# Kernel tuning notes

Measured on AMD Instinct MI355X. Metric: run time of the kernel, lower is better.

Reference implementation:

```python
import jax, jax.numpy as jnp
import numpy as np

B, S, D, H = 2, 2048, 1024, 16
HD = D // H  # 64
SOFT_CAP = 50.0
MAX_WAVELENGTH = 10000.0


def apply_rope(x, positions, head_dim):
    # x: [B,S,H,hd], positions: [B,S]
    fraction = 2.0 * jnp.arange(head_dim // 2, dtype=jnp.float32) / head_dim
    timescale = MAX_WAVELENGTH ** fraction                      # [hd/2]
    sinusoid = positions.astype(jnp.float32)[..., None] / timescale  # [B,S,hd/2]
    sin = jnp.sin(sinusoid)[..., None, :]                       # [B,S,1,hd/2]
    cos = jnp.cos(sinusoid)[..., None, :]
    first, second = jnp.split(x, 2, axis=-1)
    out = jnp.concatenate(
        [first * cos - second * sin, second * cos + first * sin], axis=-1)
    return out.astype(x.dtype)


def setup_inputs() -> dict:
    key = jax.random.key(0)
    k1, k2, k3 = jax.random.split(key, 3)
    inputs = jax.random.normal(k1, (B, S, D), jnp.float32)
    segment_positions = jnp.tile(jnp.arange(S, dtype=jnp.int32), (B, 1))
    mask = jnp.tril(jnp.ones((S, S), dtype=bool))[None, None]   # causal [1,1,S,S]
    w_in = jax.random.normal(k2, (D, H, 3 * HD), jnp.float32) * 0.02
    w_out = jax.random.normal(k3, (H, HD, D), jnp.float32) * 0.02
    return {"inputs": inputs, "segment_positions": segment_positions,
            "mask": mask, "w_in": w_in, "w_out": w_out}


def reference(inputs, segment_positions, mask, w_in, w_out):
    # fused QKV projection: [B,S,H,3*hd]
    proj = jnp.einsum('bsd,dhe->bshe', inputs, w_in)
    q, k, v = jnp.split(proj, 3, axis=-1)
    q = apply_rope(q, segment_positions, HD)
    k = apply_rope(k, segment_positions, HD)
    q = q / jnp.sqrt(jnp.float32(HD))
    attn = jnp.einsum('bqhd,bkhd->bhqk', q, k)                  # [B,H,S,S]
    big_neg = jnp.finfo(jnp.float32).min
    attn = jnp.where(mask, attn, big_neg)
    attn = jnp.tanh(attn / SOFT_CAP) * SOFT_CAP                 # soft-cap AFTER mask
    attn = jax.nn.softmax(attn, axis=-1)
    x = jnp.einsum('bhqk,bkhd->bqhd', attn, v)
    return jnp.einsum('bqhd,hdo->bqo', x, w_out)
```

## Files before the change

### kernel.cpp

```cpp
#include <hip/hip_runtime.h>
#include <math.h>

#define BB 2
#define SS 2048
#define DD 1024
#define HH 16
#define HDIM 64
#define BS (BB*SS)
#define NQKV (HH*3*HDIM)
#define PERHEAD ((size_t)SS*HDIM)

typedef __attribute__((ext_vector_type(8))) short bf16x8;
typedef __attribute__((ext_vector_type(4))) short bf16x4;
typedef __attribute__((ext_vector_type(4))) float f32x4;

typedef const __attribute__((address_space(1))) unsigned int ga_u32;
typedef __attribute__((address_space(3))) unsigned int lds_u32;

__device__ inline short f2bf(float x) {
    union { float f; unsigned u; } v; v.f = x;
    unsigned r = v.u + 0x7FFF + ((v.u >> 16) & 1);
    return (short)(r >> 16);
}

__device__ inline void gl_lds16(const void* g, void* l) {
    __builtin_amdgcn_global_load_lds((ga_u32*)g, (lds_u32*)l, 16, 0, 0);
}

__device__ inline f32x4 mfma16(bf16x4 a, bf16x4 b, f32x4 c) {
#if __has_builtin(__builtin_amdgcn_mfma_f32_16x16x16bf16_1k)
    return __builtin_amdgcn_mfma_f32_16x16x16bf16_1k(a, b, c, 0, 0, 0);
#else
    f32x4 d;
    asm("v_mfma_f32_16x16x16_bf16 %0, %1, %2, %3"
        : "=v"(d) : "v"(a), "v"(b), "v"(c));
    return d;
#endif
}

__global__ __launch_bounds__(256)
void prep_kernel(const float* __restrict__ A, unsigned short* __restrict__ Ab,
                 const int* __restrict__ pos, float2* __restrict__ tab)
{
    int bid = blockIdx.x, t = threadIdx.x;
    if (bid < 4096) {
        int i = (bid * 256 + t) * 4;
        float4 v = *(const float4*)&A[i];
        ushort4 o;
        o.x = (unsigned short)f2bf(v.x); o.y = (unsigned short)f2bf(v.y);
        o.z = (unsigned short)f2bf(v.z); o.w = (unsigned short)f2bf(v.w);
        *(ushort4*)&Ab[i] = o;
    } else {
        int idx = (bid - 4096) * 256 + t;
        int i = idx & 31, s = (idx >> 5) & 2047, b = idx >> 16;
        float p  = (float)pos[b * SS + s];
        float ts = powf(10000.0f, (float)i / 32.0f);
        float sn, cs;
        sincosf(p / ts, &sn, &cs);
        tab[idx] = make_float2(cs, sn);
    }
}

__global__ __launch_bounds__(256)
void transpose2_bf16(const float* __restrict__ Win, unsigned short* __restrict__ Wtin,
                     const float* __restrict__ Wout, unsigned short* __restrict__ Wtout)
{
    __shared__ float tile[64][65];
    int id = blockIdx.x;
    const float* W; unsigned short* Wt; int K, N, tx, ty;
    if (id < 768) { W = Win;  Wt = Wtin;  K = DD; N = NQKV; tx = id % 48; ty = id / 48; }
    else { id -= 768; W = Wout; Wt = Wtout; K = DD; N = DD;  tx = id % 16; ty = id / 16; }
    const int k0 = ty * 64, n0 = tx * 64;
    const int t = threadIdx.x;
    #pragma unroll
    for (int i = 0; i < 4; ++i) {
        int lin = t + 256 * i;
        int r = lin >> 4, c4 = (lin & 15) << 2;
        float4 v = *(const float4*)&W[(size_t)(k0 + r) * N + n0 + c4];
        tile[r][c4] = v.x; tile[r][c4 + 1] = v.y;
        tile[r][c4 + 2] = v.z; tile[r][c4 + 3] = v.w;
    }
    __syncthreads();
    #pragma unroll
    for (int i = 0; i < 4; ++i) {
        int lin = t + 256 * i;
        int n = lin >> 4, c4 = (lin & 15) << 2;
        ushort4 o;
        o.x = (unsigned short)f2bf(tile[c4 + 0][n]);
        o.y = (unsigned short)f2bf(tile[c4 + 1][n]);
        o.z = (unsigned short)f2bf(tile[c4 + 2][n]);
        o.w = (unsigned short)f2bf(tile[c4 + 3][n]);
        *(ushort4*)&Wt[(size_t)(n0 + n) * K + k0 + c4] = o;
    }
}

template<int QKV, int NT>
__global__ __launch_bounds__(256)
void gemm_mfma(const unsigned short* __restrict__ A,
               const unsigned short* __restrict__ Bt,
               float* __restrict__ C,
               unsigned short* __restrict__ Qb, unsigned short* __restrict__ Kb,
               unsigned short* __restrict__ Vb,
               const float2* __restrict__ tab,
               int M, int N, int K)
{
    __shared__ __align__(16) unsigned short As[128 * 32];
    __shared__ __align__(16) unsigned short Bs[NT * 32 * 32];
    const int t = threadIdx.x;
    const int wave = t >> 6, lane = t & 63;
    const int quad = lane >> 4, lc = lane & 15;
    const int bm = blockIdx.y * 128, bn = blockIdx.x * (NT * 32);
    const int wr = wave >> 1, wc = wave & 1;

    const int cb   = blockIdx.x * 2 + wc;
    const int h    = QKV ? (cb / 3) : 0;
    const int part = QKV ? (cb % 3) : 0;
    const bool vswap = QKV && (part == 2);

    const int r4 = lane >> 2;
    const int sc = (lane & 3) ^ ((lane >> 3) & 3);
    const unsigned short* aptr0 = A + (size_t)(bm + wave * 32 + r4) * K + sc * 8;
    const unsigned short* aptr1 = aptr0 + (size_t)16 * K;
    unsigned short* alds0 = &As[(wave * 32) * 32];
    unsigned short* alds1 = alds0 + 16 * 32;
    const unsigned short* bptr0 = Bt + (size_t)(bn + wave * (NT * 8) + r4) * K + sc * 8;
    const unsigned short* bptr1 = bptr0 + (size_t)16 * K;
    unsigned short* blds0 = &Bs[(wave * (NT * 8)) * 32];
    unsigned short* blds1 = blds0 + 16 * 32;

    const int cx = quad ^ ((lc >> 1) & 3);

    f32x4 acc[4][NT] = {};

    for (int k0 = 0; k0 < K; k0 += 32) {
        gl_lds16(aptr0 + k0, alds0);
        gl_lds16(aptr1 + k0, alds1);
        gl_lds16(bptr0 + k0, blds0);
        if (NT == 4) gl_lds16(bptr1 + k0, blds1);
        __syncthreads();

        bf16x8 af[4], bfr[NT];
        #pragma unroll
        for (int rt = 0; rt < 4; ++rt)
            af[rt] = *(const bf16x8*)&As[(wr * 64 + rt * 16 + lc) * 32 + cx * 8];
        #pragma unroll
        for (int nt = 0; nt < NT; ++nt)
            bfr[nt] = *(const bf16x8*)&Bs[(wc * (NT * 16) + nt * 16 + lc) * 32 + cx * 8];
        if (vswap) {
            #pragma unroll
            for (int rt = 0; rt < 4; ++rt)
                #pragma unroll
                for (int nt = 0; nt < NT; ++nt)
                    acc[rt][nt] = __builtin_amdgcn_mfma_f32_16x16x32_bf16(
                        bfr[nt], af[rt], acc[rt][nt], 0, 0, 0);
        } else {
            #pragma unroll
            for (int rt = 0; rt < 4; ++rt)
                #pragma unroll
                for (int nt = 0; nt < NT; ++nt)
                    acc[rt][nt] = __builtin_amdgcn_mfma_f32_16x16x32_bf16(
                        af[rt], bfr[nt], acc[rt][nt], 0, 0, 0);
        }
        __syncthreads();
    }

    if (QKV) {
        if (part == 2) {
            #pragma unroll
            for (int rt = 0; rt < 4; ++rt) {
                int m = bm + wr * 64 + rt * 16 + lc;
                int b = m >> 11, s = m & 2047;
                #pragma unroll
                for (int nt = 0; nt < 4; ++nt) {
                    #pragma unroll
                    for (int reg = 0; reg < 4; ++reg) {
                        int hd = nt * 16 + quad * 4 + reg;
                        Vb[(((size_t)(b * HH + h)) * HDIM + hd) * SS + s] =
                            (unsigned short)f2bf(acc[rt][nt][reg]);
                    }
                }
            }
        } else {
            unsigned short* dst = part == 0 ? Qb : Kb;
            const float scale = part == 0 ? 0.125f : 1.0f;
            #pragma unroll
            for (int rt = 0; rt < 4; ++rt) {
                #pragma unroll
                for (int reg = 0; reg < 4; ++reg) {
                    int m = bm + wr * 64 + rt * 16 + quad * 4 + reg;
                    int b = m >> 11, s = m & 2047;
                    size_t rowbase = (((size_t)(b * HH + h)) * SS + s) * HDIM;
                    #pragma unroll
                    for (int nt = 0; nt < 2; ++nt) {
                        int i = nt * 16 + lc;
                        float2 cssn = tab[((size_t)(b * SS + s)) * 32 + i];
                        float first  = acc[rt][nt][reg];
                        float second = acc[rt][nt + 2][reg];
                        dst[rowbase + i] =
                            (unsigned short)f2bf((first * cssn.x - second * cssn.y) * scale);
                        dst[rowbase + i + 32] =
                            (unsigned short)f2bf((second * cssn.x + first * cssn.y) * scale);
                    }
                }
            }
        }
    } else {
        #pragma unroll
        for (int rt = 0; rt < 4; ++rt)
            #pragma unroll
            for (int reg = 0; reg < 4; ++reg) {
                int m = bm + wr * 64 + rt * 16 + quad * 4 + reg;
                #pragma unroll
                for (int nt = 0; nt < NT; ++nt) {
                    int n = bn + wc * (NT * 16) + nt * 16 + lc;
                    C[(size_t)m * N + n] = acc[rt][nt][reg];
                }
            }
    }
}

__global__ __launch_bounds__(256)
void attn_mfma_kernel(const unsigned short* __restrict__ Qb,
                      const unsigned short* __restrict__ Kb,
                      const unsigned short* __restrict__ Vb,
                      unsigned short* __restrict__ Xb)
{
    __shared__ __align__(16) unsigned short Ks[2][64 * 64];
    __shared__ __align__(16) unsigned short Vs[2][64 * 64];

    const int t    = threadIdx.x;
    const int wave = t >> 6, lane = t & 63;
    const int quad = lane >> 4, lc = lane & 15;
    const int qt   = 31 - (blockIdx.x >> 5);
    const int bh   = blockIdx.x & 31;
    const int b    = bh >> 4, h = bh & 15;

    const unsigned short* Kbase = Kb + (size_t)bh * PERHEAD;
    const unsigned short* Vbase = Vb + (size_t)bh * PERHEAD;

    const int r8 = lane >> 3, c8 = lane & 7, gcs = c8 ^ r8;

    const unsigned short* Qbase =
        Qb + ((size_t)bh * SS + (size_t)(qt * 64 + wave * 16)) * HDIM;
    bf16x8 qf[2];
    qf[0] = *(const bf16x8*)&Qbase[lc * HDIM + quad * 8];
    qf[1] = *(const bf16x8*)&Qbase[lc * HDIM + 32 + quad * 8];

    f32x4 O[4] = {{0,0,0,0},{0,0,0,0},{0,0,0,0},{0,0,0,0}};
    float l = 0.0f;

    {
        const unsigned short* ks = Kbase + (size_t)(wave * 16 + r8) * HDIM + gcs * 8;
        gl_lds16(ks,            &Ks[0][(wave * 16)     * 64]);
        gl_lds16(ks + 8 * HDIM, &Ks[0][(wave * 16 + 8) * 64]);
        const unsigned short* vs = Vbase + (size_t)(wave * 16 + r8) * SS + gcs * 8;
        gl_lds16(vs,          &Vs[0][(wave * 16)     * 64]);
        gl_lds16(vs + 8 * SS, &Vs[0][(wave * 16 + 8) * 64]);
    }

    for (int kt = 0; kt <= qt; ++kt) {
        __syncthreads();
        const int buf = kt & 1;
        if (kt < qt) {
            const int nb = buf ^ 1;
            const unsigned short* ks =
                Kbase + (size_t)((kt + 1) * 64 + wave * 16 + r8) * HDIM + gcs * 8;
            gl_lds16(ks,            &Ks[nb][(wave * 16)     * 64]);
            gl_lds16(ks + 8 * HDIM, &Ks[nb][(wave * 16 + 8) * 64]);
            const unsigned short* vs =
                Vbase + (size_t)(wave * 16 + r8) * SS + (kt + 1) * 64 + gcs * 8;
            gl_lds16(vs,          &Vs[nb][(wave * 16)     * 64]);
            gl_lds16(vs + 8 * SS, &Vs[nb][(wave * 16 + 8) * 64]);
        }

        f32x4 St[4];
        #pragma unroll
        for (int kg = 0; kg < 4; ++kg) {
            St[kg] = (f32x4){0.f, 0.f, 0.f, 0.f};
            #pragma unroll
            for (int khd = 0; khd < 2; ++khd) {
                int pc = ((khd << 2) | quad) ^ (lc & 7);
                bf16x8 kf = *(const bf16x8*)&Ks[buf][(kg * 16 + lc) * 64 + pc * 8];
                St[kg] = __builtin_amdgcn_mfma_f32_16x16x32_bf16(
                    kf, qf[khd], St[kg], 0, 0, 0);
            }
        }

        const bool diag = (kt == qt);
        bf16x4 pf[4];
        #pragma unroll
        for (int kg = 0; kg < 4; ++kg) {
            #pragma unroll
            for (int reg = 0; reg < 4; ++reg) {
                float s  = St[kg][reg];
                float s2 = s * s;
                float u  = fmaf(s2 * s, -1.92359246e-4f, s * 1.44269504f);
                float p  = __builtin_amdgcn_exp2f(u);
                if (diag && (kg * 16 + quad * 4 + reg > wave * 16 + lc)) p = 0.f;
                l += p;
                pf[kg][reg] = f2bf(p);
            }
        }

        #pragma unroll
        for (int g = 0; g < 4; ++g) {
            #pragma unroll
            for (int kg = 0; kg < 4; ++kg) {
                int pc2 = (kg * 2 + (quad >> 1)) ^ (lc & 7);
                bf16x4 vf = *(const bf16x4*)
                    &Vs[buf][(g * 16 + lc) * 64 + pc2 * 8 + (quad & 1) * 4];
                O[g] = mfma16(pf[kg], vf, O[g]);
            }
        }
    }

    l += __shfl_xor(l, 16);
    l += __shfl_xor(l, 32);
    #pragma unroll
    for (int reg = 0; reg < 4; ++reg) {
        float lq  = __shfl(l, quad * 4 + reg);
        float inv = __builtin_amdgcn_rcpf(lq);
        int q_g = qt * 64 + wave * 16 + quad * 4 + reg;
        size_t base = ((size_t)b * SS + q_g) * DD + h * HDIM;
        #pragma unroll
        for (int g = 0; g < 4; ++g)
            Xb[base + g * 16 + lc] = (unsigned short)f2bf(O[g][reg] * inv);
    }
}

extern "C" void kernel_launch(void* const* d_in, const int* in_sizes, int n_in,
                              void* d_out, int out_size, void* d_ws, size_t ws_size,
                              hipStream_t stream)
{
    const float* inputs = (const float*)d_in[0];
    const int*   pos    = (const int*)d_in[1];
    const float* w_in   = (const float*)d_in[3];
    const float* w_out  = (const float*)d_in[4];
    float* out = (float*)d_out;

    const size_t NELT = (size_t)BB * HH * SS * HDIM;
    unsigned short* Ab     = (unsigned short*)d_ws;
    unsigned short* Wt_in  = Ab + NELT;
    unsigned short* Wt_out = Wt_in + (size_t)NQKV * DD;
    unsigned short* Qb     = Wt_out + (size_t)DD * DD;
    unsigned short* Kb     = Qb + NELT;
    unsigned short* Vb     = Kb + NELT;
    unsigned short* Xb     = Vb + NELT;
    float2*         tab    = (float2*)(Xb + NELT);

    dim3 blk(256);
    prep_kernel<<<dim3(4096 + 512), blk, 0, stream>>>(inputs, Ab, pos, tab);
    transpose2_bf16<<<dim3(1024), blk, 0, stream>>>(w_in, Wt_in, w_out, Wt_out);
    gemm_mfma<1, 4><<<dim3(NQKV / 128, BS / 128), blk, 0, stream>>>(
        Ab, Wt_in, nullptr, Qb, Kb, Vb, tab, BS, NQKV, DD);
    attn_mfma_kernel<<<dim3(32 * BB * HH), blk, 0, stream>>>(Qb, Kb, Vb, Xb);
    gemm_mfma<0, 2><<<dim3(DD / 64, BS / 128), blk, 0, stream>>>(
        Xb, Wt_out, out, nullptr, nullptr, nullptr, nullptr, BS, DD, DD);
}
```

Before: 191.1 us.

## Merge prep kernels and compute softmax row sums via MFMA in attention

Folds the weight transpose kernel into the input-conversion/rope-table kernel, saving one launch. In the attention inner loop, the bf16 conversion becomes a round-half-up plus byte-permute pack, and the softmax denominator is accumulated with an MFMA against a ones vector instead of scalar adds and cross-lane shuffles. The denominator now sums the bf16-rounded probabilities, which matches the values fed to the PV product. The merged setup kernel reserves shared memory for every block, including the conversion blocks that do not use it, which may lower their occupancy.

After: 188.0 us (median of 2 runs). About the same (-1.6%).

```diff
diff --git a/kernel.cpp b/kernel.cpp
--- a/kernel.cpp
+++ b/kernel.cpp
@@ -39,9 +39,12 @@
 }
 
 __global__ __launch_bounds__(256)
-void prep_kernel(const float* __restrict__ A, unsigned short* __restrict__ Ab,
-                 const int* __restrict__ pos, float2* __restrict__ tab)
+void setup_kernel(const float* __restrict__ A, unsigned short* __restrict__ Ab,
+                  const int* __restrict__ pos, float2* __restrict__ tab,
+                  const float* __restrict__ Win, unsigned short* __restrict__ Wtin,
+                  const float* __restrict__ Wout, unsigned short* __restrict__ Wtout)
 {
+    __shared__ float tile[64][65];
     int bid = blockIdx.x, t = threadIdx.x;
     if (bid < 4096) {
         int i = (bid * 256 + t) * 4;
@@ -50,7 +53,9 @@
         o.x = (unsigned short)f2bf(v.x); o.y = (unsigned short)f2bf(v.y);
         o.z = (unsigned short)f2bf(v.z); o.w = (unsigned short)f2bf(v.w);
         *(ushort4*)&Ab[i] = o;
-    } else {
+        return;
+    }
+    if (bid < 4608) {
         int idx = (bid - 4096) * 256 + t;
         int i = idx & 31, s = (idx >> 5) & 2047, b = idx >> 16;
         float p  = (float)pos[b * SS + s];
@@ -58,20 +63,12 @@
         float sn, cs;
         sincosf(p / ts, &sn, &cs);
         tab[idx] = make_float2(cs, sn);
-    }
-}
-
-__global__ __launch_bounds__(256)
-void transpose2_bf16(const float* __restrict__ Win, unsigned short* __restrict__ Wtin,
-                     const float* __restrict__ Wout, unsigned short* __restrict__ Wtout)
-{
-    __shared__ float tile[64][65];
-    int id = blockIdx.x;
+        return;
+    }
     const float* W; unsigned short* Wt; int K, N, tx, ty;
-    if (id < 768) { W = Win;  Wt = Wtin;  K = DD; N = NQKV; tx = id % 48; ty = id / 48; }
-    else { id -= 768; W = Wout; Wt = Wtout; K = DD; N = DD;  tx = id % 16; ty = id / 16; }
+    if (bid < 5376) { int id = bid - 4608; W = Win;  Wt = Wtin;  K = DD; N = NQKV; tx = id % 48; ty = id / 48; }
+    else            { int id = bid - 5376; W = Wout; Wt = Wtout; K = DD; N = DD;   tx = id % 16; ty = id / 16; }
     const int k0 = ty * 64, n0 = tx * 64;
-    const int t = threadIdx.x;
     #pragma unroll
     for (int i = 0; i < 4; ++i) {
         int lin = t + 256 * i;
@@ -247,7 +244,8 @@
     qf[1] = *(const bf16x8*)&Qbase[lc * HDIM + 32 + quad * 8];
 
     f32x4 O[4] = {{0,0,0,0},{0,0,0,0},{0,0,0,0},{0,0,0,0}};
-    float l = 0.0f;
+    f32x4 l_acc = {0.f, 0.f, 0.f, 0.f};
+    const bf16x4 ones4 = {(short)0x3F80, (short)0x3F80, (short)0x3F80, (short)0x3F80};
 
     {
         const unsigned short* ks = Kbase + (size_t)(wave * 16 + r8) * HDIM + gcs * 8;
@@ -290,16 +288,21 @@
         bf16x4 pf[4];
         #pragma unroll
         for (int kg = 0; kg < 4; ++kg) {
+            unsigned up[4];
             #pragma unroll
             for (int reg = 0; reg < 4; ++reg) {
                 float s  = St[kg][reg];
                 float s2 = s * s;
-                float u  = fmaf(s2 * s, -1.92359246e-4f, s * 1.44269504f);
+                float u  = s * fmaf(s2, -1.92359339e-4f, 1.44269504f);
                 float p  = __builtin_amdgcn_exp2f(u);
                 if (diag && (kg * 16 + quad * 4 + reg > wave * 16 + lc)) p = 0.f;
-                l += p;
-                pf[kg][reg] = f2bf(p);
-            }
+                up[reg] = __builtin_bit_cast(unsigned, p) + 0x8000u;
+            }
+            uint2 pk;
+            pk.x = __builtin_amdgcn_perm(up[1], up[0], 0x07060302);
+            pk.y = __builtin_amdgcn_perm(up[3], up[2], 0x07060302);
+            pf[kg] = __builtin_bit_cast(bf16x4, pk);
+            l_acc = mfma16(pf[kg], ones4, l_acc);
         }
 
         #pragma unroll
@@ -314,12 +317,9 @@
         }
     }
 
-    l += __shfl_xor(l, 16);
-    l += __shfl_xor(l, 32);
     #pragma unroll
     for (int reg = 0; reg < 4; ++reg) {
-        float lq  = __shfl(l, quad * 4 + reg);
-        float inv = __builtin_amdgcn_rcpf(lq);
+        float inv = __builtin_amdgcn_rcpf(l_acc[reg]);
         int q_g = qt * 64 + wave * 16 + quad * 4 + reg;
         size_t base = ((size_t)b * SS + q_g) * DD + h * HDIM;
         #pragma unroll
@@ -349,8 +349,8 @@
     float2*         tab    = (float2*)(Xb + NELT);
 
     dim3 blk(256);
-    prep_kernel<<<dim3(4096 + 512), blk, 0, stream>>>(inputs, Ab, pos, tab);
-    transpose2_bf16<<<dim3(1024), blk, 0, stream>>>(w_in, Wt_in, w_out, Wt_out);
+    setup_kernel<<<dim3(5632), blk, 0, stream>>>(
+        inputs, Ab, pos, tab, w_in, Wt_in, w_out, Wt_out);
     gemm_mfma<1, 4><<<dim3(NQKV / 128, BS / 128), blk, 0, stream>>>(
         Ab, Wt_in, nullptr, Qb, Kb, Vb, tab, BS, NQKV, DD);
     attn_mfma_kernel<<<dim3(32 * BB * HH), blk, 0, stream>>>(Qb, Kb, Vb, Xb);
```
